# Performance work log

Measured on AMD Instinct MI355X. Metric: run time of the kernel, lower is better.

The kernel has to match this reference:

```python
import jax, jax.numpy as jnp
import numpy as np
from jax import lax

N, CI, CO, H, W = 2, 256, 256, 64, 64
K, G, DIL, PAD, STRIDE = 3, 8, 1, 1, 1
P = K * K
CG = CO // G  # group channels = 32


def setup_inputs() -> dict:
    key = jax.random.key(0)
    ks = jax.random.split(key, 24)
    r = lambda i, shape, s=1.0: jax.random.normal(ks[i], shape, jnp.float32) * s
    u = lambda i, shape: jax.random.uniform(ks[i], shape, jnp.float32, 0.5, 1.5)
    return dict(
        x=r(0, (N, CI, H, W)),
        conv1_w=r(1, (CO, CI), CI ** -0.5),
        bn1_g=u(2, (CO,)), bn1_b=r(3, (CO,), 0.1), bn1_m=r(4, (CO,), 0.1), bn1_v=u(5, (CO,)),
        inproj_w=r(6, (CO, CO), CO ** -0.5), inproj_b=r(7, (CO,), 0.02),
        dw_w=r(8, (CO, 1, K, K), 0.2), dw_b=r(9, (CO,), 0.02),
        ln_g=u(10, (CO,)), ln_b=r(11, (CO,), 0.02),
        off_w=r(12, (CO, G * P * 2), CO ** -0.5), off_b=jnp.zeros((G * P * 2,), jnp.float32),
        mask_w=r(13, (CO, G * P), CO ** -0.5), mask_b=jnp.zeros((G * P,), jnp.float32),
        outproj_w=r(14, (CO, CO), CO ** -0.5), outproj_b=r(15, (CO,), 0.02),
        bn2_g=u(16, (CO,)), bn2_b=r(17, (CO,), 0.1), bn2_m=r(18, (CO,), 0.1), bn2_v=u(19, (CO,)),
    )


def _bn(x, g, b, m, v, eps):
    # inference-mode BatchNorm2d on NCHW
    return (x - m[:, None, None]) * (g[:, None, None] * lax.rsqrt(v[:, None, None] + eps)) + b[:, None, None]


def _dcn_core(t, offset, mask):
    # t: (N,H,W,C) projected input; offset: (N,H,W,G*P*2); mask: (N,H,W,G,P) softmaxed
    xp = jnp.pad(t, ((0, 0), (PAD, PAD), (PAD, PAD), (0, 0)))
    H_, W_ = H + 2 * PAD, W + 2 * PAD
    # reference points (sample centers), normalized to padded size
    ry = ((DIL * (K - 1)) / 2 + 0.5 + STRIDE * jnp.arange(H, dtype=t.dtype)) / H_
    rx = ((DIL * (K - 1)) / 2 + 0.5 + STRIDE * jnp.arange(W, dtype=t.dtype)) / W_
    base = (DIL * (K - 1)) // 2
    gx = jnp.linspace(-base, -base + (K - 1) * DIL, K, dtype=t.dtype) / W_
    gy = jnp.linspace(-base, -base + (K - 1) * DIL, K, dtype=t.dtype) / H_
    gxx, gyy = jnp.meshgrid(gx, gy, indexing='ij')  # x varies along axis 0 (torch meshgrid order)
    grid = jnp.stack([gxx, gyy], -1).reshape(P, 2)  # (P,2)
    off = offset.reshape(N, H, W, G, P, 2) / jnp.array([W_, H_], t.dtype)
    loc_x = rx[None, None, :, None, None] + grid[:, 0][None, None, None, None] + off[..., 0]  # (N,H,W,G,P)
    loc_y = ry[None, :, None, None, None] + grid[:, 1][None, None, None, None] + off[..., 1]
    # grid_sample(align_corners=False): pixel = norm*size - 0.5
    px = jnp.transpose(loc_x * W_ - 0.5, (0, 3, 1, 2, 4)).reshape(N, G, H * W * P)
    py = jnp.transpose(loc_y * H_ - 0.5, (0, 3, 1, 2, 4)).reshape(N, G, H * W * P)
    # grouped channels-last image: (N,G,H_*W_,CG)
    xg = jnp.transpose(xp.reshape(N, H_, W_, G, CG), (0, 3, 1, 2, 4)).reshape(N, G, H_ * W_, CG)
    x0 = jnp.floor(px)
    y0 = jnp.floor(py)
    wx1 = px - x0
    wy1 = py - y0
    x0i = x0.astype(jnp.int32)
    y0i = y0.astype(jnp.int32)

    def corner(xi, yi, w):
        valid = (xi >= 0) & (xi <= W_ - 1) & (yi >= 0) & (yi <= H_ - 1)
        idx = jnp.clip(yi, 0, H_ - 1) * W_ + jnp.clip(xi, 0, W_ - 1)
        v = jnp.take_along_axis(xg, idx[..., None], axis=2)  # (N,G,M,CG)
        return v * jnp.where(valid, w, 0.0)[..., None]

    sampled = (corner(x0i, y0i, (1 - wx1) * (1 - wy1))
               + corner(x0i + 1, y0i, wx1 * (1 - wy1))
               + corner(x0i, y0i + 1, (1 - wx1) * wy1)
               + corner(x0i + 1, y0i + 1, wx1 * wy1))
    sampled = sampled.reshape(N, G, H * W, P, CG)
    mg = jnp.transpose(mask, (0, 3, 1, 2, 4)).reshape(N, G, H * W, P)
    out = jnp.einsum('nglpc,nglp->nglc', sampled, mg)
    return jnp.transpose(out, (0, 2, 1, 3)).reshape(N, H, W, G * CG)


def reference(x, conv1_w, bn1_g, bn1_b, bn1_m, bn1_v, inproj_w, inproj_b, dw_w, dw_b,
              ln_g, ln_b, off_w, off_b, mask_w, mask_b, outproj_w, outproj_b,
              bn2_g, bn2_b, bn2_m, bn2_v):
    # Conv(inc, ouc, k=1): 1x1 conv (no bias) + BN(eps=1e-3) + SiLU
    y = jnp.einsum('nchw,oc->nohw', x, conv1_w)
    y = jax.nn.silu(_bn(y, bn1_g, bn1_b, bn1_m, bn1_v, 1e-3))
    t = jnp.transpose(y, (0, 2, 3, 1))  # NHWC
    xproj = t @ inproj_w + inproj_b     # input_proj Linear
    # offset/mask branch: depthwise conv (k=3,s=1,p=1) -> LN over C -> GELU
    z = lax.conv_general_dilated(y, dw_w, (1, 1), ((PAD, PAD), (PAD, PAD)),
                                 feature_group_count=CO,
                                 dimension_numbers=('NCHW', 'OIHW', 'NCHW')) + dw_b[None, :, None, None]
    z = jnp.transpose(z, (0, 2, 3, 1))
    mu = jnp.mean(z, -1, keepdims=True)
    var = jnp.var(z, -1, keepdims=True)
    z = (z - mu) * lax.rsqrt(var + 1e-5) * ln_g + ln_b
    z = jax.nn.gelu(z, approximate=False)
    offset = z @ off_w + off_b  # (N,H,W,G*P*2)
    mask = jax.nn.softmax((z @ mask_w + mask_b).reshape(N, H, W, G, P), axis=-1)
    s = _dcn_core(xproj, offset, mask)
    s = s @ outproj_w + outproj_b  # output_proj Linear
    o = jnp.transpose(s, (0, 3, 1, 2))  # back to NCHW
    return jax.nn.silu(_bn(o, bn2_g, bn2_b, bn2_m, bn2_v, 1e-5))
```

## Files before the change

### kernel.cpp

```cpp
#include <hip/hip_runtime.h>
#include <math.h>

#define CC    256
#define HH    64
#define WW    64
#define HWSZ  4096
#define NPIX  8192
#define MT    16
#define TT    16
#define ASTR  264

typedef __attribute__((ext_vector_type(8))) short short8;
typedef __attribute__((ext_vector_type(4))) float f32x4;

__device__ __forceinline__ float silu_f(float x) { return x / (1.f + __expf(-x)); }

__device__ __forceinline__ short f2bf(float f) {
    unsigned u = __float_as_uint(f);
    unsigned r = (u + 0x7fffu + ((u >> 16) & 1u)) >> 16;
    return (short)r;
}
__device__ __forceinline__ unsigned pk2(float a, float b) {
    return (unsigned)(unsigned short)f2bf(a) | ((unsigned)(unsigned short)f2bf(b) << 16);
}
__device__ __forceinline__ float4 bf4(uint2 u) {
    float4 r;
    r.x = __uint_as_float(u.x << 16);
    r.y = __uint_as_float(u.x & 0xffff0000u);
    r.z = __uint_as_float(u.y << 16);
    r.w = __uint_as_float(u.y & 0xffff0000u);
    return r;
}
__device__ __forceinline__ void bf8acc(uint4 u, float wgt, float* acc) {
    acc[0] += wgt * __uint_as_float(u.x << 16);
    acc[1] += wgt * __uint_as_float(u.x & 0xffff0000u);
    acc[2] += wgt * __uint_as_float(u.y << 16);
    acc[3] += wgt * __uint_as_float(u.y & 0xffff0000u);
    acc[4] += wgt * __uint_as_float(u.z << 16);
    acc[5] += wgt * __uint_as_float(u.z & 0xffff0000u);
    acc[6] += wgt * __uint_as_float(u.w << 16);
    acc[7] += wgt * __uint_as_float(u.w & 0xffff0000u);
}

__global__ void k_prep(const float* __restrict__ cw, const float* __restrict__ ipw,
                       const float* __restrict__ offw, const float* __restrict__ maskw,
                       const float* __restrict__ opw, const float* __restrict__ dww,
                       const float* __restrict__ offb, const float* __restrict__ maskb,
                       const float* __restrict__ g1, const float* __restrict__ b1,
                       const float* __restrict__ m1, const float* __restrict__ v1,
                       const float* __restrict__ g2, const float* __restrict__ b2,
                       const float* __restrict__ m2, const float* __restrict__ v2,
                       short* __restrict__ Wc1b, short* __restrict__ Wipb,
                       short* __restrict__ Whb, short* __restrict__ Wopb,
                       float* __restrict__ dwt,
                       float* __restrict__ bh, float* __restrict__ sc1, float* __restrict__ sh1,
                       float* __restrict__ sc2, float* __restrict__ sh2) {
    int o = blockIdx.x, c = threadIdx.x;
    Wc1b[o * CC + c] = f2bf(cw[o * CC + c]);
    Wipb[o * CC + c] = f2bf(ipw[c * CC + o]);
    float hv = 0.f;
    if (o < 144) hv = offw[c * 144 + o];
    else if (o < 216) hv = maskw[c * 72 + (o - 144)];
    Whb[o * CC + c] = f2bf(hv);
    Wopb[o * CC + c] = f2bf(opw[c * CC + o]);
    if (o < 9) dwt[o * CC + c] = dww[c * 9 + o];
    if (o == 0) {
        float bv = 0.f;
        if (c < 144) bv = offb[c];
        else if (c < 216) bv = maskb[c - 144];
        bh[c] = bv;
        float s1 = g1[c] * rsqrtf(v1[c] + 1e-3f);
        sc1[c] = s1; sh1[c] = b1[c] - m1[c] * s1;
        float s2 = g2[c] * rsqrtf(v2[c] + 1e-5f);
        sc2[c] = s2; sh2[c] = b2[c] - m2[c] * s2;
    }
}

__device__ __forceinline__ void gemm2(const short* As, const short* __restrict__ Wb,
                                      int lane, int n0, f32x4 acc[2]) {
    const int m = lane & 15, q = lane >> 4;
#pragma unroll
    for (int kk = 0; kk < 8; ++kk) {
        int c0 = kk * 32 + q * 8;
        short8 a = *(const short8*)(As + m * ASTR + c0);
#pragma unroll
        for (int nt = 0; nt < 2; ++nt) {
            short8 b = *(const short8*)(Wb + (size_t)(n0 + nt * 16 + m) * CC + c0);
            acc[nt] = __builtin_amdgcn_mfma_f32_16x16x32_bf16(a, b, acc[nt], 0, 0, 0);
        }
    }
}

__global__ __launch_bounds__(512, 4) void k_conv_in(
        const float* __restrict__ x, const short* __restrict__ Wc1b,
        const short* __restrict__ Wipb, const float* __restrict__ sc1,
        const float* __restrict__ sh1, const float* __restrict__ ipb,
        short* __restrict__ ybf, short* __restrict__ xpb) {
    __shared__ __align__(16) short As[MT * ASTR];
    int tid = threadIdx.x, lane = tid & 63, wv = tid >> 6;
    int pix0 = blockIdx.x * MT;
    int n = pix0 >> 12, hw0 = pix0 & (HWSZ - 1);
    int n0 = wv * 32;
    const float* xn = x + (size_t)n * CC * HWSZ;
#pragma unroll
    for (int rep = 0; rep < 2; ++rep) {
        int f = tid + rep * 512;
        int c = f >> 2, i4 = (f & 3) * 4;
        float4 v = *(const float4*)(xn + (size_t)c * HWSZ + hw0 + i4);
        As[(i4 + 0) * ASTR + c] = f2bf(v.x);
        As[(i4 + 1) * ASTR + c] = f2bf(v.y);
        As[(i4 + 2) * ASTR + c] = f2bf(v.z);
        As[(i4 + 3) * ASTR + c] = f2bf(v.w);
    }
    __syncthreads();
    f32x4 acc[2];
    acc[0] = (f32x4){0.f, 0.f, 0.f, 0.f};
    acc[1] = (f32x4){0.f, 0.f, 0.f, 0.f};
    gemm2(As, Wc1b, lane, n0, acc);
    __syncthreads();
    int col = lane & 15, qr = (lane >> 4) * 4;
#pragma unroll
    for (int nt = 0; nt < 2; ++nt) {
        int o = n0 + nt * 16 + col;
        float sc = sc1[o], sh = sh1[o];
#pragma unroll
        for (int r = 0; r < 4; ++r) {
            int pix = qr + r;
            short vb = f2bf(silu_f(acc[nt][r] * sc + sh));
            ybf[(size_t)(pix0 + pix) * CC + o] = vb;
            As[pix * ASTR + o] = vb;
        }
    }
    __syncthreads();
    acc[0] = (f32x4){0.f, 0.f, 0.f, 0.f};
    acc[1] = (f32x4){0.f, 0.f, 0.f, 0.f};
    gemm2(As, Wipb, lane, n0, acc);
#pragma unroll
    for (int nt = 0; nt < 2; ++nt) {
        int o = n0 + nt * 16 + col;
        float bo = ipb[o];
#pragma unroll
        for (int r = 0; r < 4; ++r)
            xpb[(size_t)(pix0 + qr + r) * CC + o] = f2bf(acc[nt][r] + bo);
    }
}

__global__ __launch_bounds__(512, 4) void k_tail(
        const short* __restrict__ ybf, const short* __restrict__ xpb,
        const float* __restrict__ dwt, const float* __restrict__ dwb,
        const float* __restrict__ lng, const float* __restrict__ lnb,
        const short* __restrict__ Whb, const float* __restrict__ bh,
        const short* __restrict__ Wopb, const float* __restrict__ opb,
        const float* __restrict__ sc2, const float* __restrict__ sh2,
        float* __restrict__ out) {
    __shared__ __align__(16) short As[TT * ASTR];
    __shared__ __align__(16) float buf[TT * 260];
    float* ml   = buf;
    float* loff = buf + 1216;
    float* xs   = buf;

    int tid = threadIdx.x, lane = tid & 63, wv = tid >> 6;
    int pix0 = blockIdx.x * TT;
    int n = pix0 >> 12, hw0 = pix0 & (HWSZ - 1);
    int h = hw0 >> 6, w0 = hw0 & 63;
    int c0 = lane * 4;
    int n0 = wv * 32;
    int col = lane & 15, qr = (lane >> 4) * 4;

    {
        float4 dwbv = *(const float4*)(dwb + c0);
        float4 lngv = *(const float4*)(lng + c0);
        float4 lnbv = *(const float4*)(lnb + c0);
        const short* yn = ybf + (size_t)n * HWSZ * CC;
#pragma unroll
        for (int i = 0; i < 2; ++i) {
            int pix = wv * 2 + i;
            int w = w0 + pix;
            float4 acc = dwbv;
#pragma unroll
            for (int ky = 0; ky < 3; ++ky) {
                int yy = h + ky - 1;
                int yc = min(max(yy, 0), HH - 1);
                float vy = (yy == yc) ? 1.f : 0.f;
#pragma unroll
                for (int kx = 0; kx < 3; ++kx) {
                    int xx = w + kx - 1;
                    int xc = min(max(xx, 0), WW - 1);
                    float vm = vy * ((xx == xc) ? 1.f : 0.f);
                    int t = ky * 3 + kx;
                    float4 wt = *(const float4*)(dwt + t * CC + c0);
                    float4 yv = bf4(*(const uint2*)(yn + (size_t)((yc << 6) + xc) * CC + c0));
                    acc.x += yv.x * wt.x * vm;
                    acc.y += yv.y * wt.y * vm;
                    acc.z += yv.z * wt.z * vm;
                    acc.w += yv.w * wt.w * vm;
                }
            }
            float s1 = acc.x + acc.y + acc.z + acc.w;
            float s2 = acc.x * acc.x + acc.y * acc.y + acc.z * acc.z + acc.w * acc.w;
#pragma unroll
            for (int off = 32; off > 0; off >>= 1) {
                s1 += __shfl_xor(s1, off);
                s2 += __shfl_xor(s2, off);
            }
            float mu = s1 * (1.f / 256.f);
            float var = s2 * (1.f / 256.f) - mu * mu;
            float rs = rsqrtf(var + 1e-5f);
            float4 zv;
            zv.x = (acc.x - mu) * rs * lngv.x + lnbv.x;
            zv.y = (acc.y - mu) * rs * lngv.y + lnbv.y;
            zv.z = (acc.z - mu) * rs * lngv.z + lnbv.z;
            zv.w = (acc.w - mu) * rs * lngv.w + lnbv.w;
            zv.x = 0.5f * zv.x * (1.f + erff(zv.x * 0.70710678118654752f));
            zv.y = 0.5f * zv.y * (1.f + erff(zv.y * 0.70710678118654752f));
            zv.z = 0.5f * zv.z * (1.f + erff(zv.z * 0.70710678118654752f));
            zv.w = 0.5f * zv.w * (1.f + erff(zv.w * 0.70710678118654752f));
            *(uint2*)(As + pix * ASTR + c0) = make_uint2(pk2(zv.x, zv.y), pk2(zv.z, zv.w));
        }
    }
    __syncthreads();

    {
        f32x4 acc[2];
        acc[0] = (f32x4){0.f, 0.f, 0.f, 0.f};
        acc[1] = (f32x4){0.f, 0.f, 0.f, 0.f};
        gemm2(As, Whb, lane, n0, acc);
#pragma unroll
        for (int nt = 0; nt < 2; ++nt) {
            int o = n0 + nt * 16 + col;
            float bo = bh[o];
#pragma unroll
            for (int r = 0; r < 4; ++r) {
                float v = acc[nt][r] + bo;
                int pix = qr + r;
                if (o < 144) loff[pix * 144 + o] = v;
                else if (o < 216) ml[pix * 76 + (o - 144)] = v;
            }
        }
    }
    __syncthreads();

    {
        int ph = lane >> 5;
        int g  = (lane >> 2) & 7;
        int ci = lane & 3;
        int gc0 = g * 32 + ci * 8;
        int pix = wv * 2 + ph;
        int w = w0 + pix;
        float e9[9];
        {
            const float* row = ml + pix * 76 + g * 9;
            float mx = -1e30f;
#pragma unroll
            for (int p = 0; p < 9; ++p) { e9[p] = row[p]; mx = fmaxf(mx, e9[p]); }
            float ssum = 0.f;
#pragma unroll
            for (int p = 0; p < 9; ++p) { e9[p] = __expf(e9[p] - mx); ssum += e9[p]; }
            float inv = 1.f / ssum;
#pragma unroll
            for (int p = 0; p < 9; ++p) e9[p] *= inv;
        }
        const float* lp = loff + pix * 144 + g * 18;
        const short* xpn = xpb + (size_t)n * HWSZ * CC;
        float acc8[8];
#pragma unroll
        for (int k = 0; k < 8; ++k) acc8[k] = 0.f;
#pragma unroll
        for (int p = 0; p < 9; ++p) {
            float ox = lp[p * 2], oy = lp[p * 2 + 1];
            float px = (float)(w + p / 3) + ox;
            float py = (float)(h + p % 3) + oy;
            float fx = floorf(px), fy = floorf(py);
            float wx1 = px - fx, wy1 = py - fy;
            int x0 = (int)fx, y0 = (int)fy;
            int x1 = x0 + 1, y1 = y0 + 1;
            int xc0 = min(max(x0, 1), WW), xc1 = min(max(x1, 1), WW);
            int yc0 = min(max(y0, 1), HH), yc1 = min(max(y1, 1), HH);
            float vx0 = (x0 == xc0) ? 1.f : 0.f, vx1 = (x1 == xc1) ? 1.f : 0.f;
            float vy0 = (y0 == yc0) ? 1.f : 0.f, vy1 = (y1 == yc1) ? 1.f : 0.f;
            float mval = e9[p];
            float w00 = (1.f - wx1) * (1.f - wy1) * mval * vx0 * vy0;
            float w10 = wx1 * (1.f - wy1) * mval * vx1 * vy0;
            float w01 = (1.f - wx1) * wy1 * mval * vx0 * vy1;
            float w11 = wx1 * wy1 * mval * vx1 * vy1;
            uint4 u00 = *(const uint4*)(xpn + (size_t)(((yc0 - 1) << 6) + (xc0 - 1)) * CC + gc0);
            uint4 u10 = *(const uint4*)(xpn + (size_t)(((yc0 - 1) << 6) + (xc1 - 1)) * CC + gc0);
            uint4 u01 = *(const uint4*)(xpn + (size_t)(((yc1 - 1) << 6) + (xc0 - 1)) * CC + gc0);
            uint4 u11 = *(const uint4*)(xpn + (size_t)(((yc1 - 1) << 6) + (xc1 - 1)) * CC + gc0);
            bf8acc(u00, w00, acc8);
            bf8acc(u10, w10, acc8);
            bf8acc(u01, w01, acc8);
            bf8acc(u11, w11, acc8);
        }
        uint4 pkv;
        pkv.x = pk2(acc8[0], acc8[1]);
        pkv.y = pk2(acc8[2], acc8[3]);
        pkv.z = pk2(acc8[4], acc8[5]);
        pkv.w = pk2(acc8[6], acc8[7]);
        *(uint4*)(As + pix * ASTR + gc0) = pkv;
    }
    __syncthreads();

    {
        f32x4 acc[2];
        acc[0] = (f32x4){0.f, 0.f, 0.f, 0.f};
        acc[1] = (f32x4){0.f, 0.f, 0.f, 0.f};
        gemm2(As, Wopb, lane, n0, acc);
#pragma unroll
        for (int nt = 0; nt < 2; ++nt) {
            int o = n0 + nt * 16 + col;
            float bo = opb[o], sc = sc2[o], sh = sh2[o];
#pragma unroll
            for (int r = 0; r < 4; ++r)
                xs[(qr + r) * 260 + o] = silu_f((acc[nt][r] + bo) * sc + sh);
        }
    }
    __syncthreads();

    {
        int i4 = (tid & 3) * 4;
        int obase = tid >> 2;
        float* on = out + (size_t)n * CC * HWSZ + hw0 + i4;
#pragma unroll
        for (int pass = 0; pass < 2; ++pass) {
            int o = obase + pass * 128;
            float4 ov;
            ov.x = xs[(i4 + 0) * 260 + o];
            ov.y = xs[(i4 + 1) * 260 + o];
            ov.z = xs[(i4 + 2) * 260 + o];
            ov.w = xs[(i4 + 3) * 260 + o];
            *(float4*)(on + (size_t)o * HWSZ) = ov;
        }
    }
}

extern "C" void kernel_launch(void* const* d_in, const int* in_sizes, int n_in,
                              void* d_out, int out_size, void* d_ws, size_t ws_size,
                              hipStream_t stream) {
    const float* x        = (const float*)d_in[0];
    const float* conv1_w  = (const float*)d_in[1];
    const float* bn1_g    = (const float*)d_in[2];
    const float* bn1_b    = (const float*)d_in[3];
    const float* bn1_m    = (const float*)d_in[4];
    const float* bn1_v    = (const float*)d_in[5];
    const float* inproj_w = (const float*)d_in[6];
    const float* inproj_b = (const float*)d_in[7];
    const float* dw_w     = (const float*)d_in[8];
    const float* dw_b     = (const float*)d_in[9];
    const float* ln_g     = (const float*)d_in[10];
    const float* ln_b     = (const float*)d_in[11];
    const float* off_w    = (const float*)d_in[12];
    const float* off_b    = (const float*)d_in[13];
    const float* mask_w   = (const float*)d_in[14];
    const float* mask_b   = (const float*)d_in[15];
    const float* outproj_w = (const float*)d_in[16];
    const float* outproj_b = (const float*)d_in[17];
    const float* bn2_g    = (const float*)d_in[18];
    const float* bn2_b    = (const float*)d_in[19];
    const float* bn2_m    = (const float*)d_in[20];
    const float* bn2_v    = (const float*)d_in[21];
    float* out = (float*)d_out;

    short* Wc1b = (short*)d_ws;
    short* Wipb = Wc1b + 65536;
    short* Whb  = Wipb + 65536;
    short* Wopb = Whb + 65536;
    float* fp   = (float*)(Wopb + 65536);
    float* dwt  = fp;
    float* bh   = dwt + 9 * CC;
    float* sc1  = bh + 256;
    float* sh1  = sc1 + 256;
    float* sc2  = sh1 + 256;
    float* sh2  = sc2 + 256;
    short* ybf  = (short*)(sh2 + 256);
    short* xpb  = ybf + (size_t)NPIX * CC;

    k_prep<<<dim3(CC), dim3(CC), 0, stream>>>(conv1_w, inproj_w, off_w, mask_w, outproj_w, dw_w,
                                              off_b, mask_b, bn1_g, bn1_b, bn1_m, bn1_v,
                                              bn2_g, bn2_b, bn2_m, bn2_v,
                                              Wc1b, Wipb, Whb, Wopb, dwt, bh, sc1, sh1, sc2, sh2);
    k_conv_in<<<dim3(NPIX / MT), dim3(512), 0, stream>>>(x, Wc1b, Wipb, sc1, sh1, inproj_b, ybf, xpb);
    k_tail<<<dim3(NPIX / TT), dim3(512), 0, stream>>>(ybf, xpb, dwt, dw_b, ln_g, ln_b,
                                                      Whb, bh, Wopb, outproj_b, sc2, sh2, out);
}
```

Before: 153.8 us.

## Double block size to 1024 threads, one 16-column MFMA tile per wave

New measurement: 158.0 us. 2.7% more time.

```diff
diff --git a/kernel.cpp b/kernel.cpp
--- a/kernel.cpp
+++ b/kernel.cpp
@@ -31,15 +31,11 @@
     r.w = __uint_as_float(u.y & 0xffff0000u);
     return r;
 }
-__device__ __forceinline__ void bf8acc(uint4 u, float wgt, float* acc) {
+__device__ __forceinline__ void bf4acc(uint2 u, float wgt, float* acc) {
     acc[0] += wgt * __uint_as_float(u.x << 16);
     acc[1] += wgt * __uint_as_float(u.x & 0xffff0000u);
     acc[2] += wgt * __uint_as_float(u.y << 16);
     acc[3] += wgt * __uint_as_float(u.y & 0xffff0000u);
-    acc[4] += wgt * __uint_as_float(u.z << 16);
-    acc[5] += wgt * __uint_as_float(u.z & 0xffff0000u);
-    acc[6] += wgt * __uint_as_float(u.w << 16);
-    acc[7] += wgt * __uint_as_float(u.w & 0xffff0000u);
 }
 
 __global__ void k_prep(const float* __restrict__ cw, const float* __restrict__ ipw,
@@ -76,22 +72,19 @@
     }
 }
 
-__device__ __forceinline__ void gemm2(const short* As, const short* __restrict__ Wb,
-                                      int lane, int n0, f32x4 acc[2]) {
+__device__ __forceinline__ void gemm1(const short* As, const short* __restrict__ Wb,
+                                      int lane, int n0, f32x4* acc) {
     const int m = lane & 15, q = lane >> 4;
 #pragma unroll
     for (int kk = 0; kk < 8; ++kk) {
         int c0 = kk * 32 + q * 8;
         short8 a = *(const short8*)(As + m * ASTR + c0);
-#pragma unroll
-        for (int nt = 0; nt < 2; ++nt) {
-            short8 b = *(const short8*)(Wb + (size_t)(n0 + nt * 16 + m) * CC + c0);
-            acc[nt] = __builtin_amdgcn_mfma_f32_16x16x32_bf16(a, b, acc[nt], 0, 0, 0);
-        }
-    }
-}
-
-__global__ __launch_bounds__(512, 4) void k_conv_in(
+        short8 b = *(const short8*)(Wb + (size_t)(n0 + m) * CC + c0);
+        *acc = __builtin_amdgcn_mfma_f32_16x16x32_bf16(a, b, *acc, 0, 0, 0);
+    }
+}
+
+__global__ __launch_bounds__(1024, 8) void k_conv_in(
         const float* __restrict__ x, const short* __restrict__ Wc1b,
         const short* __restrict__ Wipb, const float* __restrict__ sc1,
         const float* __restrict__ sh1, const float* __restrict__ ipb,
@@ -100,12 +93,10 @@
     int tid = threadIdx.x, lane = tid & 63, wv = tid >> 6;
     int pix0 = blockIdx.x * MT;
     int n = pix0 >> 12, hw0 = pix0 & (HWSZ - 1);
-    int n0 = wv * 32;
+    int n0 = wv * 16;
     const float* xn = x + (size_t)n * CC * HWSZ;
-#pragma unroll
-    for (int rep = 0; rep < 2; ++rep) {
-        int f = tid + rep * 512;
-        int c = f >> 2, i4 = (f & 3) * 4;
+    {
+        int c = tid >> 2, i4 = (tid & 3) * 4;
         float4 v = *(const float4*)(xn + (size_t)c * HWSZ + hw0 + i4);
         As[(i4 + 0) * ASTR + c] = f2bf(v.x);
         As[(i4 + 1) * ASTR + c] = f2bf(v.y);
@@ -113,39 +104,31 @@
         As[(i4 + 3) * ASTR + c] = f2bf(v.w);
     }
     __syncthreads();
-    f32x4 acc[2];
-    acc[0] = (f32x4){0.f, 0.f, 0.f, 0.f};
-    acc[1] = (f32x4){0.f, 0.f, 0.f, 0.f};
-    gemm2(As, Wc1b, lane, n0, acc);
+    f32x4 acc = (f32x4){0.f, 0.f, 0.f, 0.f};
+    gemm1(As, Wc1b, lane, n0, &acc);
     __syncthreads();
     int col = lane & 15, qr = (lane >> 4) * 4;
-#pragma unroll
-    for (int nt = 0; nt < 2; ++nt) {
-        int o = n0 + nt * 16 + col;
+    int o = n0 + col;
+    {
         float sc = sc1[o], sh = sh1[o];
 #pragma unroll
-        for (int r = 0; r < 4; ++r) {
-            int pix = qr + r;
-            short vb = f2bf(silu_f(acc[nt][r] * sc + sh));
-            ybf[(size_t)(pix0 + pix) * CC + o] = vb;
-            As[pix * ASTR + o] = vb;
-        }
-    }
-    __syncthreads();
-    acc[0] = (f32x4){0.f, 0.f, 0.f, 0.f};
-    acc[1] = (f32x4){0.f, 0.f, 0.f, 0.f};
-    gemm2(As, Wipb, lane, n0, acc);
-#pragma unroll
-    for (int nt = 0; nt < 2; ++nt) {
-        int o = n0 + nt * 16 + col;
+        for (int r = 0; r < 4; ++r)
+            As[(qr + r) * ASTR + o] = f2bf(silu_f(acc[r] * sc + sh));
+    }
+    __syncthreads();
+    *(uint2*)(ybf + (size_t)(pix0 + wv) * CC + lane * 4) =
+        *(const uint2*)(As + wv * ASTR + lane * 4);
+    acc = (f32x4){0.f, 0.f, 0.f, 0.f};
+    gemm1(As, Wipb, lane, n0, &acc);
+    {
         float bo = ipb[o];
 #pragma unroll
         for (int r = 0; r < 4; ++r)
-            xpb[(size_t)(pix0 + qr + r) * CC + o] = f2bf(acc[nt][r] + bo);
-    }
-}
-
-__global__ __launch_bounds__(512, 4) void k_tail(
+            xpb[(size_t)(pix0 + qr + r) * CC + o] = f2bf(acc[r] + bo);
+    }
+}
+
+__global__ __launch_bounds__(1024, 8) void k_tail(
         const short* __restrict__ ybf, const short* __restrict__ xpb,
         const float* __restrict__ dwt, const float* __restrict__ dwb,
         const float* __restrict__ lng, const float* __restrict__ lnb,
@@ -164,7 +147,7 @@
     int n = pix0 >> 12, hw0 = pix0 & (HWSZ - 1);
     int h = hw0 >> 6, w0 = hw0 & 63;
     int c0 = lane * 4;
-    int n0 = wv * 32;
+    int n0 = wv * 16;
     int col = lane & 15, qr = (lane >> 4) * 4;
 
     {
@@ -172,80 +155,71 @@
         float4 lngv = *(const float4*)(lng + c0);
         float4 lnbv = *(const float4*)(lnb + c0);
         const short* yn = ybf + (size_t)n * HWSZ * CC;
-#pragma unroll
-        for (int i = 0; i < 2; ++i) {
-            int pix = wv * 2 + i;
-            int w = w0 + pix;
-            float4 acc = dwbv;
-#pragma unroll
-            for (int ky = 0; ky < 3; ++ky) {
-                int yy = h + ky - 1;
-                int yc = min(max(yy, 0), HH - 1);
-                float vy = (yy == yc) ? 1.f : 0.f;
-#pragma unroll
-                for (int kx = 0; kx < 3; ++kx) {
-                    int xx = w + kx - 1;
-                    int xc = min(max(xx, 0), WW - 1);
-                    float vm = vy * ((xx == xc) ? 1.f : 0.f);
-                    int t = ky * 3 + kx;
-                    float4 wt = *(const float4*)(dwt + t * CC + c0);
-                    float4 yv = bf4(*(const uint2*)(yn + (size_t)((yc << 6) + xc) * CC + c0));
-                    acc.x += yv.x * wt.x * vm;
-                    acc.y += yv.y * wt.y * vm;
-                    acc.z += yv.z * wt.z * vm;
-                    acc.w += yv.w * wt.w * vm;
-                }
+        int pix = wv;
+        int w = w0 + pix;
+        float4 acc = dwbv;
+#pragma unroll
+        for (int ky = 0; ky < 3; ++ky) {
+            int yy = h + ky - 1;
+            int yc = min(max(yy, 0), HH - 1);
+            float vy = (yy == yc) ? 1.f : 0.f;
+#pragma unroll
+            for (int kx = 0; kx < 3; ++kx) {
+                int xx = w + kx - 1;
+                int xc = min(max(xx, 0), WW - 1);
+                float vm = vy * ((xx == xc) ? 1.f : 0.f);
+                int t = ky * 3 + kx;
+                float4 wt = *(const float4*)(dwt + t * CC + c0);
+                float4 yv = bf4(*(const uint2*)(yn + (size_t)((yc << 6) + xc) * CC + c0));
+                acc.x += yv.x * wt.x * vm;
+                acc.y += yv.y * wt.y * vm;
+                acc.z += yv.z * wt.z * vm;
+                acc.w += yv.w * wt.w * vm;
             }
-            float s1 = acc.x + acc.y + acc.z + acc.w;
-            float s2 = acc.x * acc.x + acc.y * acc.y + acc.z * acc.z + acc.w * acc.w;
-#pragma unroll
-            for (int off = 32; off > 0; off >>= 1) {
-                s1 += __shfl_xor(s1, off);
-                s2 += __shfl_xor(s2, off);
-            }
-            float mu = s1 * (1.f / 256.f);
-            float var = s2 * (1.f / 256.f) - mu * mu;
-            float rs = rsqrtf(var + 1e-5f);
-            float4 zv;
-            zv.x = (acc.x - mu) * rs * lngv.x + lnbv.x;
-            zv.y = (acc.y - mu) * rs * lngv.y + lnbv.y;
-            zv.z = (acc.z - mu) * rs * lngv.z + lnbv.z;
-            zv.w = (acc.w - mu) * rs * lngv.w + lnbv.w;
-            zv.x = 0.5f * zv.x * (1.f + erff(zv.x * 0.70710678118654752f));
-            zv.y = 0.5f * zv.y * (1.f + erff(zv.y * 0.70710678118654752f));
-            zv.z = 0.5f * zv.z * (1.f + erff(zv.z * 0.70710678118654752f));
-            zv.w = 0.5f * zv.w * (1.f + erff(zv.w * 0.70710678118654752f));
-            *(uint2*)(As + pix * ASTR + c0) = make_uint2(pk2(zv.x, zv.y), pk2(zv.z, zv.w));
-        }
-    }
-    __syncthreads();
-
-    {
-        f32x4 acc[2];
-        acc[0] = (f32x4){0.f, 0.f, 0.f, 0.f};
-        acc[1] = (f32x4){0.f, 0.f, 0.f, 0.f};
-        gemm2(As, Whb, lane, n0, acc);
-#pragma unroll
-        for (int nt = 0; nt < 2; ++nt) {
-            int o = n0 + nt * 16 + col;
-            float bo = bh[o];
-#pragma unroll
-            for (int r = 0; r < 4; ++r) {
-                float v = acc[nt][r] + bo;
-                int pix = qr + r;
-                if (o < 144) loff[pix * 144 + o] = v;
-                else if (o < 216) ml[pix * 76 + (o - 144)] = v;
-            }
-        }
-    }
-    __syncthreads();
-
-    {
-        int ph = lane >> 5;
-        int g  = (lane >> 2) & 7;
-        int ci = lane & 3;
-        int gc0 = g * 32 + ci * 8;
-        int pix = wv * 2 + ph;
+        }
+        float s1 = acc.x + acc.y + acc.z + acc.w;
+        float s2 = acc.x * acc.x + acc.y * acc.y + acc.z * acc.z + acc.w * acc.w;
+#pragma unroll
+        for (int off = 32; off > 0; off >>= 1) {
+            s1 += __shfl_xor(s1, off);
+            s2 += __shfl_xor(s2, off);
+        }
+        float mu = s1 * (1.f / 256.f);
+        float var = s2 * (1.f / 256.f) - mu * mu;
+        float rs = rsqrtf(var + 1e-5f);
+        float4 zv;
+        zv.x = (acc.x - mu) * rs * lngv.x + lnbv.x;
+        zv.y = (acc.y - mu) * rs * lngv.y + lnbv.y;
+        zv.z = (acc.z - mu) * rs * lngv.z + lnbv.z;
+        zv.w = (acc.w - mu) * rs * lngv.w + lnbv.w;
+        zv.x = 0.5f * zv.x * (1.f + erff(zv.x * 0.70710678118654752f));
+        zv.y = 0.5f * zv.y * (1.f + erff(zv.y * 0.70710678118654752f));
+        zv.z = 0.5f * zv.z * (1.f + erff(zv.z * 0.70710678118654752f));
+        zv.w = 0.5f * zv.w * (1.f + erff(zv.w * 0.70710678118654752f));
+        *(uint2*)(As + pix * ASTR + c0) = make_uint2(pk2(zv.x, zv.y), pk2(zv.z, zv.w));
+    }
+    __syncthreads();
+
+    {
+        f32x4 acc = (f32x4){0.f, 0.f, 0.f, 0.f};
+        gemm1(As, Whb, lane, n0, &acc);
+        int o = n0 + col;
+        float bo = bh[o];
+#pragma unroll
+        for (int r = 0; r < 4; ++r) {
+            float v = acc[r] + bo;
+            int pix = qr + r;
+            if (o < 144) loff[pix * 144 + o] = v;
+            else if (o < 216) ml[pix * 76 + (o - 144)] = v;
+        }
+    }
+    __syncthreads();
+
+    {
+        int g  = lane >> 3;
+        int ci = lane & 7;
+        int gc0 = g * 32 + ci * 4;
+        int pix = wv;
         int w = w0 + pix;
         float e9[9];
         {
@@ -262,9 +236,9 @@
         }
         const float* lp = loff + pix * 144 + g * 18;
         const short* xpn = xpb + (size_t)n * HWSZ * CC;
-        float acc8[8];
-#pragma unroll
-        for (int k = 0; k < 8; ++k) acc8[k] = 0.f;
+        float acc4[4];
+#pragma unroll
+        for (int k = 0; k < 4; ++k) acc4[k] = 0.f;
 #pragma unroll
         for (int p = 0; p < 9; ++p) {
             float ox = lp[p * 2], oy = lp[p * 2 + 1];
@@ -283,54 +257,41 @@
             float w10 = wx1 * (1.f - wy1) * mval * vx1 * vy0;
             float w01 = (1.f - wx1) * wy1 * mval * vx0 * vy1;
             float w11 = wx1 * wy1 * mval * vx1 * vy1;
-            uint4 u00 = *(const uint4*)(xpn + (size_t)(((yc0 - 1) << 6) + (xc0 - 1)) * CC + gc0);
-            uint4 u10 = *(const uint4*)(xpn + (size_t)(((yc0 - 1) << 6) + (xc1 - 1)) * CC + gc0);
-            uint4 u01 = *(const uint4*)(xpn + (size_t)(((yc1 - 1) << 6) + (xc0 - 1)) * CC + gc0);
-            uint4 u11 = *(const uint4*)(xpn + (size_t)(((yc1 - 1) << 6) + (xc1 - 1)) * CC + gc0);
-            bf8acc(u00, w00, acc8);
-            bf8acc(u10, w10, acc8);
-            bf8acc(u01, w01, acc8);
-            bf8acc(u11, w11, acc8);
-        }
-        uint4 pkv;
-        pkv.x = pk2(acc8[0], acc8[1]);
-        pkv.y = pk2(acc8[2], acc8[3]);
-        pkv.z = pk2(acc8[4], acc8[5]);
-        pkv.w = pk2(acc8[6], acc8[7]);
-        *(uint4*)(As + pix * ASTR + gc0) = pkv;
-    }
-    __syncthreads();
-
-    {
-        f32x4 acc[2];
-        acc[0] = (f32x4){0.f, 0.f, 0.f, 0.f};
-        acc[1] = (f32x4){0.f, 0.f, 0.f, 0.f};
-        gemm2(As, Wopb, lane, n0, acc);
-#pragma unroll
-        for (int nt = 0; nt < 2; ++nt) {
-            int o = n0 + nt * 16 + col;
-            float bo = opb[o], sc = sc2[o], sh = sh2[o];
-#pragma unroll
-            for (int r = 0; r < 4; ++r)
-                xs[(qr + r) * 260 + o] = silu_f((acc[nt][r] + bo) * sc + sh);
-        }
+            uint2 u00 = *(const uint2*)(xpn + (size_t)(((yc0 - 1) << 6) + (xc0 - 1)) * CC + gc0);
+            uint2 u10 = *(const uint2*)(xpn + (size_t)(((yc0 - 1) << 6) + (xc1 - 1)) * CC + gc0);
+            uint2 u01 = *(const uint2*)(xpn + (size_t)(((yc1 - 1) << 6) + (xc0 - 1)) * CC + gc0);
+            uint2 u11 = *(const uint2*)(xpn + (size_t)(((yc1 - 1) << 6) + (xc1 - 1)) * CC + gc0);
+            bf4acc(u00, w00, acc4);
+            bf4acc(u10, w10, acc4);
+            bf4acc(u01, w01, acc4);
+            bf4acc(u11, w11, acc4);
+        }
+        *(uint2*)(As + pix * ASTR + gc0) =
+            make_uint2(pk2(acc4[0], acc4[1]), pk2(acc4[2], acc4[3]));
+    }
+    __syncthreads();
+
+    {
+        f32x4 acc = (f32x4){0.f, 0.f, 0.f, 0.f};
+        gemm1(As, Wopb, lane, n0, &acc);
+        int o = n0 + col;
+        float bo = opb[o], sc = sc2[o], sh = sh2[o];
+#pragma unroll
+        for (int r = 0; r < 4; ++r)
+            xs[(qr + r) * 260 + o] = silu_f((acc[r] + bo) * sc + sh);
     }
     __syncthreads();
 
     {
         int i4 = (tid & 3) * 4;
-        int obase = tid >> 2;
+        int o = tid >> 2;
         float* on = out + (size_t)n * CC * HWSZ + hw0 + i4;
-#pragma unroll
-        for (int pass = 0; pass < 2; ++pass) {
-            int o = obase + pass * 128;
-            float4 ov;
-            ov.x = xs[(i4 + 0) * 260 + o];
-            ov.y = xs[(i4 + 1) * 260 + o];
-            ov.z = xs[(i4 + 2) * 260 + o];
-            ov.w = xs[(i4 + 3) * 260 + o];
-            *(float4*)(on + (size_t)o * HWSZ) = ov;
-        }
+        float4 ov;
+        ov.x = xs[(i4 + 0) * 260 + o];
+        ov.y = xs[(i4 + 1) * 260 + o];
+        ov.z = xs[(i4 + 2) * 260 + o];
+        ov.w = xs[(i4 + 3) * 260 + o];
+        *(float4*)(on + (size_t)o * HWSZ) = ov;
     }
 }
 
@@ -379,7 +340,7 @@
                                               off_b, mask_b, bn1_g, bn1_b, bn1_m, bn1_v,
                                               bn2_g, bn2_b, bn2_m, bn2_v,
                                               Wc1b, Wipb, Whb, Wopb, dwt, bh, sc1, sh1, sc2, sh2);
-    k_conv_in<<<dim3(NPIX / MT), dim3(512), 0, stream>>>(x, Wc1b, Wipb, sc1, sh1, inproj_b, ybf, xpb);
-    k_tail<<<dim3(NPIX / TT), dim3(512), 0, stream>>>(ybf, xpb, dwt, dw_b, ln_g, ln_b,
-                                                      Whb, bh, Wopb, outproj_b, sc2, sh2, out);
-}
+    k_conv_in<<<dim3(NPIX / MT), dim3(1024), 0, stream>>>(x, Wc1b, Wipb, sc1, sh1, inproj_b, ybf, xpb);
+    k_tail<<<dim3(NPIX / TT), dim3(1024), 0, stream>>>(ybf, xpb, dwt, dw_b, ln_g, ln_b,
+                                                       Whb, bh, Wopb, outproj_b, sc2, sh2, out);
+}
```
